# Optimization experiments

Measured on AMD Instinct MI355X. Metric: run time of the kernel, lower is better.

Reference implementation:

```python
import jax, jax.numpy as jnp
import numpy as np

BERT = 178  # BERT_VECTOR_SIZE
WLEN = 20   # letters per word (dim1 = WLEN + BERT)


def _lstm(x, h0, c0, Wih, Whh, bih, bhh):
    """PyTorch-convention LSTM (gate order i,f,g,o). x: [B,T,D] -> outputs [B,T,H]."""
    xg = jnp.einsum('btd,gd->btg', x, Wih) + bih + bhh  # precompute input projections

    def step(carry, xt):
        h, c = carry
        g = xt + h @ Whh.T
        i, f, gg, o = jnp.split(g, 4, axis=-1)
        c = jax.nn.sigmoid(f) * c + jax.nn.sigmoid(i) * jnp.tanh(gg)
        h = jax.nn.sigmoid(o) * jnp.tanh(c)
        return (h, c), h

    _, hs = jax.lax.scan(step, (h0, c0), jnp.swapaxes(xg, 0, 1))
    return jnp.swapaxes(hs, 0, 1)  # [B,T,H]


def setup_inputs() -> dict:
    key = jax.random.key(0)
    ks = jax.random.split(key, 32)
    B, S, L = 32, 64, 50          # batch, sentence_length, number_of_letters
    Hs, Hm, D, O = 128, 256, 128, 32  # secondary_hidden, main_hidden, word_dims, output_size
    NW = B * S
    T = WLEN + BERT
    Din = D + BERT                # sentence LSTM input size = 306
    s = 0.05
    rn = lambda k, sh: jax.random.normal(k, sh, dtype=jnp.float32)
    return {
        'X': rn(ks[0], (B, S, T, L)),
        'h0w': rn(ks[1], (NW, Hs)), 'c0w': rn(ks[2], (NW, Hs)),
        'h0f': rn(ks[3], (B, Hm)), 'c0f': rn(ks[4], (B, Hm)),
        'h0b': rn(ks[5], (B, Hm)), 'c0b': rn(ks[6], (B, Hm)),
        'Wih_w': rn(ks[7], (4 * Hs, L)) * s, 'Whh_w': rn(ks[8], (4 * Hs, Hs)) * s,
        'bih_w': rn(ks[9], (4 * Hs,)) * s, 'bhh_w': rn(ks[10], (4 * Hs,)) * s,
        'Wl': rn(ks[11], (D, Hs)) * s, 'bl': rn(ks[12], (D,)) * s,
        'Wih_f': rn(ks[13], (4 * Hm, Din)) * s, 'Whh_f': rn(ks[14], (4 * Hm, Hm)) * s,
        'bih_f': rn(ks[15], (4 * Hm,)) * s, 'bhh_f': rn(ks[16], (4 * Hm,)) * s,
        'Wih_b': rn(ks[17], (4 * Hm, Din)) * s, 'Whh_b': rn(ks[18], (4 * Hm, Hm)) * s,
        'bih_b': rn(ks[19], (4 * Hm,)) * s, 'bhh_b': rn(ks[20], (4 * Hm,)) * s,
        'Wo': rn(ks[21], (O, 2 * Hm)) * s, 'bo': rn(ks[22], (O,)) * s,
    }


def reference(X, h0w, c0w, h0f, c0f, h0b, c0b,
              Wih_w, Whh_w, bih_w, bhh_w, Wl, bl,
              Wih_f, Whh_f, bih_f, bhh_f,
              Wih_b, Whh_b, bih_b, bhh_b, Wo, bo):
    B, S = X.shape[0], X.shape[1]
    L = X.shape[-1]
    NW = B * S
    Xw = X.reshape(NW, -1, L)            # [NW, WLEN+BERT, L]
    letters = Xw[:, :WLEN, :]            # [NW, WLEN, L]
    bert = Xw[:, -BERT:, 0]              # vectorized replacement of the double loop

    out_w = _lstm(letters, h0w, c0w, Wih_w, Whh_w, bih_w, bhh_w)
    word_rep = out_w[:, -1, :] @ Wl.T + bl        # [NW, D]
    word_rep = jnp.concatenate([word_rep, bert], axis=1)  # [NW, D+BERT]
    sentences = word_rep.reshape(B, S, -1)

    out_f = _lstm(sentences, h0f, c0f, Wih_f, Whh_f, bih_f, bhh_f)
    out_b = _lstm(sentences[:, ::-1, :], h0b, c0b, Wih_b, Whh_b, bih_b, bhh_b)[:, ::-1, :]
    out = jnp.concatenate([out_f, out_b], axis=-1)  # [B, S, 2*Hm]

    words = out.reshape(NW, -1)
    tags = words @ Wo.T + bo
    return jax.nn.softmax(tags, axis=1)
```

## Files before the change

kernel.cpp:

```cpp
#include <hip/hip_runtime.h>
#include <cstdint>
#include <cstddef>

#define DI static __device__ __forceinline__

using half_t  = _Float16;
using half2_t = __attribute__((ext_vector_type(2))) _Float16;
using half8_t = __attribute__((ext_vector_type(8))) _Float16;
using f32x4_t = __attribute__((ext_vector_type(4))) float;

DI uint32_t pack2(float a, float b){ half2_t h; h[0]=(half_t)a; h[1]=(half_t)b; return __builtin_bit_cast(uint32_t,h); }
DI uint16_t f16b(float a){ return __builtin_bit_cast(uint16_t,(half_t)a); }
DI float lo16(uint32_t u){ half2_t h=__builtin_bit_cast(half2_t,u); return (float)h[0]; }
DI float hi16(uint32_t u){ half2_t h=__builtin_bit_cast(half2_t,u); return (float)h[1]; }
DI float fdot2(uint32_t w, uint32_t x, float acc){
  return __builtin_amdgcn_fdot2(__builtin_bit_cast(half2_t,w), __builtin_bit_cast(half2_t,x), acc, false);
}
DI float sigm(float x){ return __builtin_amdgcn_rcpf(1.f + __expf(-x)); }
DI float tanhf_(float x){ return 1.f - 2.f*__builtin_amdgcn_rcpf(__expf(2.f*x)+1.f); }

#define SROW 308
#define HSTR 280

#define N0 32768
#define N1 16384
#define N2 8192
#define N3 512
#define N4 262144
#define N5 313344
#define N6 2048
#define N7 8192
#define N8 364544
#define NTOT (N0+N1+N2+N3+N4+N5+N6+N7+N8)

__global__ void k_prep(const float* __restrict__ X,
                       const float* __restrict__ Wih_w, const float* __restrict__ Whh_w,
                       const float* __restrict__ bih_w, const float* __restrict__ bhh_w,
                       const float* __restrict__ Wl,
                       const float* __restrict__ Wih_f, const float* __restrict__ Whh_f,
                       const float* __restrict__ bih_f, const float* __restrict__ bhh_f,
                       const float* __restrict__ Wih_b, const float* __restrict__ Whh_b,
                       const float* __restrict__ bih_b, const float* __restrict__ bhh_b,
                       const float* __restrict__ Wo,
                       uint32_t* __restrict__ wWsw, uint32_t* __restrict__ wWxw,
                       uint32_t* __restrict__ wWlf, float* __restrict__ wbsw,
                       uint32_t* __restrict__ wWs, uint32_t* __restrict__ wWihs,
                       float* __restrict__ wbss, uint32_t* __restrict__ wWo,
                       float* __restrict__ sent)
{
  for (int i = blockIdx.x*blockDim.x + threadIdx.x; i < NTOT; i += gridDim.x*blockDim.x) {
    int id = i;
    if (id < N0) {
      int kp = id & 63, ng = id >> 6;
      int w = ng>>6, g = (ng>>4)&3, jl = ng&15;
      const float* s = Whh_w + (size_t)(g*128 + w*16 + jl)*128 + 2*kp;
      wWsw[id] = pack2(s[0], s[1]);
    } else if ((id -= N0) < N1) {
      int kp = id & 31, ng = id >> 5;
      int w = ng>>6, g = (ng>>4)&3, jl = ng&15;
      if (kp < 25) {
        const float* s = Wih_w + (size_t)(g*128 + w*16 + jl)*50 + 2*kp;
        wWxw[id] = pack2(s[0], s[1]);
      } else wWxw[id] = 0u;
    } else if ((id -= N1) < N2) {
      int kp = id & 63, d = id >> 6;
      const float* s = Wl + (size_t)d*128 + 2*kp;
      wWlf[id] = pack2(s[0], s[1]);
    } else if ((id -= N2) < N3) {
      int g = id & 3, j = id>>2;
      wbsw[id] = bih_w[g*128+j] + bhh_w[g*128+j];
    } else if ((id -= N3) < N4) {
      int kp = id & 127, ng = (id>>7)&1023, dir = id>>17;
      int w = ng>>7, g = (ng>>5)&3, jl = ng&31;
      int row = g*256 + w*32 + jl;
      const float* s = (dir ? Whh_b : Whh_f) + (size_t)row*256 + 2*kp;
      wWs[id] = pack2(s[0], s[1]);
    } else if ((id -= N4) < N5) {
      int dir = id >= 156672; int r = id - dir*156672;
      int g = r & 3, j = (r>>2)&255, kp = r>>10;
      const float* s = (dir ? Wih_b : Wih_f) + (size_t)(g*256+j)*306 + 2*kp;
      wWihs[id] = pack2(s[0], s[1]);
    } else if ((id -= N5) < N6) {
      int g = id & 3, j = (id>>2)&255, dir = id>>10;
      int row = g*256+j;
      wbss[id] = dir ? (bih_b[row]+bhh_b[row]) : (bih_f[row]+bhh_f[row]);
    } else if ((id -= N6) < N7) {
      int o = id & 31, kp = id>>5;
      const float* s = Wo + (size_t)o*512 + 2*kp;
      wWo[id] = pack2(s[0], s[1]);
    } else { id -= N7;
      int wg = id / 178, ii = id % 178;
      sent[(size_t)wg*SROW + 128 + ii] = X[(size_t)wg*9900 + (20+ii)*50];
    }
  }
}

__global__ __launch_bounds__(512, 2) void k_word(
    const float* __restrict__ X, const float* __restrict__ h0w, const float* __restrict__ c0w,
    const uint32_t* __restrict__ wWsw, const uint32_t* __restrict__ wWxw,
    const float* __restrict__ wbsw, const uint32_t* __restrict__ wWlf,
    const float* __restrict__ bl, float* __restrict__ sent)
{
  __shared__ __align__(16) uint32_t lets[11520];
  __shared__ __align__(16) uint16_t hbuf[2][2176];
  const int tid = threadIdx.x;
  const int wave = tid >> 6, lane = tid & 63;
  const int l15 = lane & 15, l4 = lane >> 4;
  const int wg0 = blockIdx.x * 16;

  uint4 Bh[4][4], Bx[4][2];
  #pragma unroll
  for (int g = 0; g < 4; ++g) {
    int ng = wave*64 + g*16 + l15;
    #pragma unroll
    for (int Kt = 0; Kt < 4; ++Kt) Bh[g][Kt] = *(const uint4*)(wWsw + ng*64 + Kt*16 + l4*4);
    #pragma unroll
    for (int Kt = 0; Kt < 2; ++Kt) Bx[g][Kt] = *(const uint4*)(wWxw + ng*32 + Kt*16 + l4*4);
  }
  for (int i = tid; i < 11520; i += 512) {
    int c = i % 36, mt = i / 36; int m = mt & 15, t = mt >> 4;
    lets[i] = (c < 25) ? pack2(X[(size_t)(wg0+m)*9900 + t*50 + 2*c],
                               X[(size_t)(wg0+m)*9900 + t*50 + 2*c + 1]) : 0u;
  }
  for (int i = tid; i < 2048; i += 512) {
    int m = i >> 7, k = i & 127;
    hbuf[0][m*136 + k] = f16b(h0w[(size_t)(wg0+m)*128 + k]);
  }
  const float4 bs = *(const float4*)(wbsw + (wave*16 + l15)*4);
  float cr[4];
  #pragma unroll
  for (int r = 0; r < 4; ++r) cr[r] = c0w[(size_t)(wg0 + l4*4 + r)*128 + wave*16 + l15];
  __syncthreads();

  uint16_t* hc = hbuf[0];
  uint16_t* hn = hbuf[1];
  const uint16_t* lp = (const uint16_t*)lets;
  #pragma unroll 1
  for (int t = 0; t < 20; ++t) {
    f32x4_t acc[4];
    acc[0] = (f32x4_t){bs.x,bs.x,bs.x,bs.x};
    acc[1] = (f32x4_t){bs.y,bs.y,bs.y,bs.y};
    acc[2] = (f32x4_t){bs.z,bs.z,bs.z,bs.z};
    acc[3] = (f32x4_t){bs.w,bs.w,bs.w,bs.w};
    #pragma unroll
    for (int Kt = 0; Kt < 2; ++Kt) {
      uint4 av = *(const uint4*)(lp + (t*16 + l15)*72 + Kt*32 + l4*8);
      half8_t a = __builtin_bit_cast(half8_t, av);
      #pragma unroll
      for (int g = 0; g < 4; ++g)
        acc[g] = __builtin_amdgcn_mfma_f32_16x16x32_f16(a, __builtin_bit_cast(half8_t, Bx[g][Kt]), acc[g], 0,0,0);
    }
    #pragma unroll
    for (int Kt = 0; Kt < 4; ++Kt) {
      uint4 av = *(const uint4*)(hc + l15*136 + Kt*32 + l4*8);
      half8_t a = __builtin_bit_cast(half8_t, av);
      #pragma unroll
      for (int g = 0; g < 4; ++g)
        acc[g] = __builtin_amdgcn_mfma_f32_16x16x32_f16(a, __builtin_bit_cast(half8_t, Bh[g][Kt]), acc[g], 0,0,0);
    }
    #pragma unroll
    for (int r = 0; r < 4; ++r) {
      float cc = sigm(acc[1][r])*cr[r] + sigm(acc[0][r])*tanhf_(acc[2][r]);
      cr[r] = cc;
      float hh = sigm(acc[3][r])*tanhf_(cc);
      hn[(l4*4+r)*136 + wave*16 + l15] = f16b(hh);
    }
    uint16_t* tp = hc; hc = hn; hn = tp;
    __syncthreads();
  }
  uint4 Bl[4];
  #pragma unroll
  for (int Kt = 0; Kt < 4; ++Kt) Bl[Kt] = *(const uint4*)(wWlf + (wave*16 + l15)*64 + Kt*16 + l4*4);
  f32x4_t a2 = (f32x4_t){0.f,0.f,0.f,0.f};
  #pragma unroll
  for (int Kt = 0; Kt < 4; ++Kt) {
    uint4 av = *(const uint4*)(hc + l15*136 + Kt*32 + l4*8);
    a2 = __builtin_amdgcn_mfma_f32_16x16x32_f16(__builtin_bit_cast(half8_t, av),
                                                __builtin_bit_cast(half8_t, Bl[Kt]), a2, 0,0,0);
  }
  const float blv = bl[wave*16 + l15];
  #pragma unroll
  for (int r = 0; r < 4; ++r)
    sent[(size_t)(wg0 + l4*4 + r)*SROW + wave*16 + l15] = a2[r] + blv;
}

__global__ __launch_bounds__(256) void k_sxg(
    const float* __restrict__ sent, const uint32_t* __restrict__ Wihs,
    const float* __restrict__ bss, uint2* __restrict__ xgq)
{
  __shared__ uint32_t x16[153*8];
  const int tid = threadIdx.x;
  const int dir = blockIdx.x >> 8, rg = blockIdx.x & 255;
  for (int i = tid; i < 153*8; i += 256) {
    int r = i & 7, kp = i >> 3;
    int ot = rg*8 + r; int b = ot >> 6, tt = ot & 63;
    int si = dir ? (63 - tt) : tt;
    const float* s = sent + (size_t)(b*64 + si)*SROW + 2*kp;
    x16[kp*8 + r] = pack2(s[0], s[1]);
  }
  __syncthreads();
  const int j = tid;
  float acc[8][4];
  {
    const float4 b4 = *(const float4*)(bss + (dir*256 + j)*4);
    #pragma unroll
    for (int r = 0; r < 8; ++r) { acc[r][0]=b4.x; acc[r][1]=b4.y; acc[r][2]=b4.z; acc[r][3]=b4.w; }
  }
  for (int kp = 0; kp < 153; ++kp) {
    uint4 wv = *(const uint4*)(Wihs + ((size_t)(dir*153 + kp)*256 + j)*4);
    uint4 xa = *(const uint4*)(x16 + kp*8);
    uint4 xb = *(const uint4*)(x16 + kp*8 + 4);
    uint32_t wa[4] = {wv.x,wv.y,wv.z,wv.w};
    uint32_t xs[8] = {xa.x,xa.y,xa.z,xa.w,xb.x,xb.y,xb.z,xb.w};
    #pragma unroll
    for (int r = 0; r < 8; ++r)
      #pragma unroll
      for (int g = 0; g < 4; ++g) acc[r][g] = fdot2(wa[g], xs[r], acc[r][g]);
  }
  const int w = j >> 5, jh2 = (j >> 4) & 1, l15j = j & 15;
  #pragma unroll
  for (int r = 0; r < 8; ++r) {
    int ot = rg*8 + r; int b = ot >> 6, tt = ot & 63;
    int half = b >> 4, l4m = (b >> 2) & 3, rm = b & 3;
    uint2 v; v.x = pack2(acc[r][0], acc[r][1]); v.y = pack2(acc[r][2], acc[r][3]);
    size_t idx = ((((size_t)(dir*64 + tt)*2 + half)*8 + w)*2 + jh2)*256 + l15j*16 + l4m*4 + rm;
    xgq[idx] = v;
  }
}

__global__ __launch_bounds__(512, 2) void k_srec(
    const uint32_t* __restrict__ Ws, const float* __restrict__ h0f, const float* __restrict__ c0f,
    const float* __restrict__ h0b, const float* __restrict__ c0b,
    const uint2* __restrict__ xgq, uint16_t* __restrict__ outfb)
{
  extern __shared__ char smem[];
  uint16_t* h16a = (uint16_t*)(smem + 131072);
  uint16_t* h16b = h16a + 16*HSTR;
  const int tid = threadIdx.x;
  const int wave = tid >> 6, lane = tid & 63;
  const int dir = blockIdx.x >> 1, half = blockIdx.x & 1, m0 = half * 16;
  const int l15 = lane & 15, l4 = lane >> 4;

  uint4 Breg[8][6];
  #pragma unroll
  for (int Nt = 0; Nt < 8; ++Nt) {
    #pragma unroll
    for (int Kt = 0; Kt < 8; ++Kt) {
      int ng = wave*128 + Nt*16 + l15;
      int kq = Kt*16 + l4*4;
      uint4 v = *(const uint4*)(Ws + (size_t)(dir*1024 + ng)*128 + kq);
      if (Kt < 6) Breg[Nt][Kt] = v;
      else *(uint4*)(smem + (((wave*16 + Nt*2 + (Kt-6))*64 + lane)*16)) = v;
    }
  }
  {
    const float* h0 = dir ? h0b : h0f;
    for (int i = tid; i < 16*256; i += 512) {
      int m = i >> 8, k = i & 255;
      h16a[m*HSTR + k] = f16b(h0[(size_t)(m0+m)*256 + k]);
    }
  }
  float cr[2][4];
  {
    const float* c0 = dir ? c0b : c0f;
    #pragma unroll
    for (int jh = 0; jh < 2; ++jh)
      #pragma unroll
      for (int r = 0; r < 4; ++r) {
        int m = l4*4 + r, jj = wave*32 + jh*16 + l15;
        cr[jh][r] = c0[(size_t)(m0+m)*256 + jj];
      }
  }
  __syncthreads();

  const char* xb = (const char*)xgq + ((size_t)dir*4194304 + (size_t)half*32768)
                 + wave*4096 + l15*128 + l4*32;
  const int s0 = dir ? 63 : 0;
  const int sdelta = dir ? -65536 : 65536;
  char* op = (char*)outfb + (size_t)s0*65536 + half*32768 + dir*16384
           + (l4*4)*512 + wave*64 + l15*2;

  uint16_t* hc = h16a;
  uint16_t* hn = h16b;
  #pragma unroll 1
  for (int t = 0; t < 64; ++t) {
    uint4 xg0a = *(const uint4*)(xb);
    uint4 xg0b = *(const uint4*)(xb + 16);
    uint4 xg1a = *(const uint4*)(xb + 2048);
    uint4 xg1b = *(const uint4*)(xb + 2048 + 16);

    #pragma unroll
    for (int jh = 0; jh < 2; ++jh) {
      const uint4 xga = jh ? xg1a : xg0a;
      const uint4 xgb = jh ? xg1b : xg0b;
      f32x4_t acc[4];
      acc[0] = (f32x4_t){lo16(xga.x), lo16(xga.z), lo16(xgb.x), lo16(xgb.z)};
      acc[1] = (f32x4_t){hi16(xga.x), hi16(xga.z), hi16(xgb.x), hi16(xgb.z)};
      acc[2] = (f32x4_t){lo16(xga.y), lo16(xga.w), lo16(xgb.y), lo16(xgb.w)};
      acc[3] = (f32x4_t){hi16(xga.y), hi16(xga.w), hi16(xgb.y), hi16(xgb.w)};
      #pragma unroll
      for (int Kt = 0; Kt < 8; ++Kt) {
        uint4 av = *(const uint4*)(hc + l15*HSTR + Kt*32 + l4*8);
        half8_t a = __builtin_bit_cast(half8_t, av);
        #pragma unroll
        for (int g = 0; g < 4; ++g) {
          const int Nt = g*2 + jh;
          uint4 bv = (Kt < 6) ? Breg[Nt][Kt]
                   : *(const uint4*)(smem + (((wave*16 + Nt*2 + (Kt-6))*64 + lane)*16));
          acc[g] = __builtin_amdgcn_mfma_f32_16x16x32_f16(a, __builtin_bit_cast(half8_t, bv), acc[g], 0,0,0);
        }
      }
      #pragma unroll
      for (int r = 0; r < 4; ++r) {
        float gi = acc[0][r], gf = acc[1][r], gg = acc[2][r], go = acc[3][r];
        float ef = __expf(-gf), ei = __expf(-gi), eg = __expf(-2.f*gg);
        float pef = 1.f + ef, pei = 1.f + ei, peg = 1.f + eg;
        float num = cr[jh][r]*pei*peg + (1.f - eg)*pef;
        float cc  = num * __builtin_amdgcn_rcpf(pef*pei*peg);
        cr[jh][r] = cc;
        float ec = __expf(-2.f*cc), eo = __expf(-go);
        float hh = (1.f - ec) * __builtin_amdgcn_rcpf((1.f + ec)*(1.f + eo));
        uint16_t hb = f16b(hh);
        hn[(l4*4+r)*HSTR + wave*32 + jh*16 + l15] = hb;
        *(uint16_t*)(op + r*512 + jh*32) = hb;
      }
    }
    { uint16_t* tp = hc; hc = hn; hn = tp; }
    xb += 65536;
    op += sdelta;
    asm volatile("s_waitcnt lgkmcnt(0)\ns_barrier" ::: "memory");
  }
}

__global__ __launch_bounds__(256) void k_tags(
    const uint16_t* __restrict__ outfb, const uint32_t* __restrict__ Wo16,
    const float* __restrict__ bo, float* __restrict__ out)
{
  __shared__ uint32_t xr[8*256];
  const int tid = threadIdx.x;
  const int w0 = blockIdx.x * 8;
  const uint32_t* src = (const uint32_t*)outfb;
  for (int i = tid; i < 2048; i += 256) {
    int w = i >> 8, kp = i & 255;
    int widx = w0 + w;
    int s = widx & 63, q = widx >> 6;
    int half = q >> 4, m = q & 15;
    int dir = kp >> 7, wv = (kp >> 4) & 7, jh = (kp >> 3) & 1, l15h = kp & 7;
    xr[i] = src[s*16384 + half*8192 + dir*4096 + m*128 + wv*16 + jh*8 + l15h];
  }
  __syncthreads();
  const int o = tid & 31, w = tid >> 5;
  float a = bo[o];
  for (int kp = 0; kp < 256; ++kp)
    a = fdot2(Wo16[kp*32 + o], xr[w*256 + kp], a);
  float mx = a;
  #pragma unroll
  for (int off = 16; off; off >>= 1) mx = fmaxf(mx, __shfl_xor(mx, off, 32));
  float e = __expf(a - mx);
  float ssum = e;
  #pragma unroll
  for (int off = 16; off; off >>= 1) ssum += __shfl_xor(ssum, off, 32);
  out[(size_t)(w0+w)*32 + o] = e * __builtin_amdgcn_rcpf(ssum);
}

extern "C" void kernel_launch(void* const* d_in, const int* in_sizes, int n_in,
                              void* d_out, int out_size, void* d_ws, size_t ws_size,
                              hipStream_t stream) {
  const float* X     = (const float*)d_in[0];
  const float* h0w   = (const float*)d_in[1];
  const float* c0w   = (const float*)d_in[2];
  const float* h0f   = (const float*)d_in[3];
  const float* c0f   = (const float*)d_in[4];
  const float* h0b   = (const float*)d_in[5];
  const float* c0b   = (const float*)d_in[6];
  const float* Wih_w = (const float*)d_in[7];
  const float* Whh_w = (const float*)d_in[8];
  const float* bih_w = (const float*)d_in[9];
  const float* bhh_w = (const float*)d_in[10];
  const float* Wl    = (const float*)d_in[11];
  const float* bl    = (const float*)d_in[12];
  const float* Wih_f = (const float*)d_in[13];
  const float* Whh_f = (const float*)d_in[14];
  const float* bih_f = (const float*)d_in[15];
  const float* bhh_f = (const float*)d_in[16];
  const float* Wih_b = (const float*)d_in[17];
  const float* Whh_b = (const float*)d_in[18];
  const float* bih_b = (const float*)d_in[19];
  const float* bhh_b = (const float*)d_in[20];
  const float* Wo    = (const float*)d_in[21];
  const float* bo    = (const float*)d_in[22];

  char* ws = (char*)d_ws;
  uint32_t* wWsw  = (uint32_t*)(ws + 0);
  uint32_t* wWxw  = (uint32_t*)(ws + 131072);
  uint32_t* wWlf  = (uint32_t*)(ws + 196608);
  float*    wbsw  = (float*)   (ws + 229376);
  uint32_t* wWs   = (uint32_t*)(ws + 231424);
  uint32_t* wWihs = (uint32_t*)(ws + 1280000);
  float*    wbss  = (float*)   (ws + 2533376);
  uint32_t* wWo   = (uint32_t*)(ws + 2541568);
  float*    sent  = (float*)   (ws + 2574336);
  uint2*    xgq   = (uint2*)   (ws + 5097472);
  uint16_t* outfb = (uint16_t*)(ws + 13486080);

  hipFuncSetAttribute((const void*)k_srec, hipFuncAttributeMaxDynamicSharedMemorySize, 148992);

  k_prep<<<2048, 256, 0, stream>>>(X, Wih_w, Whh_w, bih_w, bhh_w, Wl, Wih_f, Whh_f, bih_f, bhh_f,
                                   Wih_b, Whh_b, bih_b, bhh_b, Wo,
                                   wWsw, wWxw, wWlf, wbsw, wWs, wWihs, wbss, wWo, sent);
  k_word<<<128, 512, 0, stream>>>(X, h0w, c0w, wWsw, wWxw, wbsw, wWlf, bl, sent);
  k_sxg<<<512, 256, 0, stream>>>(sent, wWihs, wbss, xgq);
  k_srec<<<4, 512, 148992, stream>>>(wWs, h0f, c0f, h0b, c0b, xgq, outfb);
  k_tags<<<256, 256, 0, stream>>>(outfb, wWo, bo, (float*)d_out);
}
```

Measured before the change: 308.3 us.

## Restructure sentence LSTM recurrence to four waves with 64 units each

The sentence recurrence kernel now runs 256 threads per block instead of 512, so each wave owns 64 hidden units and does four gate passes per timestep. The recurrent weight packing, the input-gate (xgq) layout and the output layout are all re-laid out to match, and k_tags reads the new output layout. Gate-input loads are interleaved with the passes to overlap global latency with the MFMA chains. The aim is cheaper per-step barriers and more per-wave work between syncs. In exchange, each SIMD has a single wave to hide latency, and register pressure is high: 96 uint4 weights are held in registers per thread, which risks spilling.

```diff
diff --git a/kernel.cpp b/kernel.cpp
--- a/kernel.cpp
+++ b/kernel.cpp
@@ -71,8 +71,8 @@
       wbsw[id] = bih_w[g*128+j] + bhh_w[g*128+j];
     } else if ((id -= N3) < N4) {
       int kp = id & 127, ng = (id>>7)&1023, dir = id>>17;
-      int w = ng>>7, g = (ng>>5)&3, jl = ng&31;
-      int row = g*256 + w*32 + jl;
+      int w = (ng>>8)&3, g = (ng>>6)&3, p = (ng>>4)&3, jl = ng&15;
+      int row = g*256 + w*64 + p*16 + jl;
       const float* s = (dir ? Whh_b : Whh_f) + (size_t)row*256 + 2*kp;
       wWs[id] = pack2(s[0], s[1]);
     } else if ((id -= N4) < N5) {
@@ -217,18 +217,19 @@
       #pragma unroll
       for (int g = 0; g < 4; ++g) acc[r][g] = fdot2(wa[g], xs[r], acc[r][g]);
   }
-  const int w = j >> 5, jh2 = (j >> 4) & 1, l15j = j & 15;
+  const int w = j >> 6, p = (j >> 4) & 3, l15j = j & 15;
   #pragma unroll
   for (int r = 0; r < 8; ++r) {
     int ot = rg*8 + r; int b = ot >> 6, tt = ot & 63;
-    int half = b >> 4, l4m = (b >> 2) & 3, rm = b & 3;
+    int half = b >> 4, m = b & 15;
+    int l4m = m >> 2, rm = m & 3;
     uint2 v; v.x = pack2(acc[r][0], acc[r][1]); v.y = pack2(acc[r][2], acc[r][3]);
-    size_t idx = ((((size_t)(dir*64 + tt)*2 + half)*8 + w)*2 + jh2)*256 + l15j*16 + l4m*4 + rm;
+    size_t idx = ((((size_t)(dir*64 + tt)*2 + half)*4 + w)*4 + p)*256 + l15j*16 + l4m*4 + rm;
     xgq[idx] = v;
   }
 }
 
-__global__ __launch_bounds__(512, 2) void k_srec(
+__global__ __launch_bounds__(256, 1) void k_srec(
     const uint32_t* __restrict__ Ws, const float* __restrict__ h0f, const float* __restrict__ c0f,
     const float* __restrict__ h0b, const float* __restrict__ c0b,
     const uint2* __restrict__ xgq, uint16_t* __restrict__ outfb)
@@ -241,95 +242,113 @@
   const int dir = blockIdx.x >> 1, half = blockIdx.x & 1, m0 = half * 16;
   const int l15 = lane & 15, l4 = lane >> 4;
 
-  uint4 Breg[8][6];
-  #pragma unroll
-  for (int Nt = 0; Nt < 8; ++Nt) {
-    #pragma unroll
-    for (int Kt = 0; Kt < 8; ++Kt) {
-      int ng = wave*128 + Nt*16 + l15;
-      int kq = Kt*16 + l4*4;
-      uint4 v = *(const uint4*)(Ws + (size_t)(dir*1024 + ng)*128 + kq);
-      if (Kt < 6) Breg[Nt][Kt] = v;
-      else *(uint4*)(smem + (((wave*16 + Nt*2 + (Kt-6))*64 + lane)*16)) = v;
-    }
-  }
+  uint4 Breg[4][4][6];
+  #pragma unroll
+  for (int g = 0; g < 4; ++g)
+    #pragma unroll
+    for (int p = 0; p < 4; ++p) {
+      int ng = wave*256 + g*64 + p*16 + l15;
+      #pragma unroll
+      for (int Kt = 0; Kt < 8; ++Kt) {
+        uint4 v = *(const uint4*)(Ws + (size_t)(dir*1024 + ng)*128 + Kt*16 + l4*4);
+        if (Kt < 6) Breg[g][p][Kt] = v;
+        else *(uint4*)(smem + (((wave*32 + (g*4+p)*2 + (Kt-6))*64 + lane)*16)) = v;
+      }
+    }
   {
     const float* h0 = dir ? h0b : h0f;
-    for (int i = tid; i < 16*256; i += 512) {
+    for (int i = tid; i < 16*256; i += 256) {
       int m = i >> 8, k = i & 255;
       h16a[m*HSTR + k] = f16b(h0[(size_t)(m0+m)*256 + k]);
     }
   }
-  float cr[2][4];
+  f32x4_t cr0, cr1, cr2, cr3;
   {
     const float* c0 = dir ? c0b : c0f;
     #pragma unroll
-    for (int jh = 0; jh < 2; ++jh)
-      #pragma unroll
-      for (int r = 0; r < 4; ++r) {
-        int m = l4*4 + r, jj = wave*32 + jh*16 + l15;
-        cr[jh][r] = c0[(size_t)(m0+m)*256 + jj];
-      }
+    for (int r = 0; r < 4; ++r) {
+      cr0[r] = c0[(size_t)(m0 + l4*4 + r)*256 + wave*64 + 0*16 + l15];
+      cr1[r] = c0[(size_t)(m0 + l4*4 + r)*256 + wave*64 + 1*16 + l15];
+      cr2[r] = c0[(size_t)(m0 + l4*4 + r)*256 + wave*64 + 2*16 + l15];
+      cr3[r] = c0[(size_t)(m0 + l4*4 + r)*256 + wave*64 + 3*16 + l15];
+    }
   }
   __syncthreads();
 
-  const char* xb = (const char*)xgq + ((size_t)dir*4194304 + (size_t)half*32768)
-                 + wave*4096 + l15*128 + l4*32;
+  const char* xb = (const char*)xgq + (size_t)dir*4194304 + half*32768
+                 + wave*8192 + l15*128 + l4*32;
   const int s0 = dir ? 63 : 0;
-  const int sdelta = dir ? -65536 : 65536;
-  char* op = (char*)outfb + (size_t)s0*65536 + half*32768 + dir*16384
-           + (l4*4)*512 + wave*64 + l15*2;
+  const int sdelta = dir ? -32768 : 32768;
+  char* op = (char*)outfb + (size_t)s0*32768 + half*16384 + dir*8192
+           + (l4*4)*512 + wave*128 + l15*2;
 
   uint16_t* hc = h16a;
   uint16_t* hn = h16b;
+
+#define XLOAD(P, XA, XB_) { XA = *(const uint4*)(xb + (P)*2048); XB_ = *(const uint4*)(xb + (P)*2048 + 16); }
+
+#define PASS(P, XA, XB_, CRV) {                                                          \
+    f32x4_t a0, a1, a2, a3;                                                              \
+    a0 = (f32x4_t){lo16(XA.x), lo16(XA.z), lo16(XB_.x), lo16(XB_.z)};                    \
+    a1 = (f32x4_t){hi16(XA.x), hi16(XA.z), hi16(XB_.x), hi16(XB_.z)};                    \
+    a2 = (f32x4_t){lo16(XA.y), lo16(XA.w), lo16(XB_.y), lo16(XB_.w)};                    \
+    a3 = (f32x4_t){hi16(XA.y), hi16(XA.w), hi16(XB_.y), hi16(XB_.w)};                    \
+    _Pragma("unroll")                                                                    \
+    for (int Kh = 0; Kh < 2; ++Kh) {                                                     \
+      uint4 av0 = *(const uint4*)(hc + l15*HSTR + (Kh*4+0)*32 + l4*8);                   \
+      uint4 av1 = *(const uint4*)(hc + l15*HSTR + (Kh*4+1)*32 + l4*8);                   \
+      uint4 av2 = *(const uint4*)(hc + l15*HSTR + (Kh*4+2)*32 + l4*8);                   \
+      uint4 av3 = *(const uint4*)(hc + l15*HSTR + (Kh*4+3)*32 + l4*8);                   \
+      _Pragma("unroll")                                                                  \
+      for (int g = 0; g < 4; ++g) {                                                      \
+        f32x4_t* ac = (g==0)?&a0:(g==1)?&a1:(g==2)?&a2:&a3;                              \
+        _Pragma("unroll")                                                                \
+        for (int Kq = 0; Kq < 4; ++Kq) {                                                 \
+          const int Kt = Kh*4 + Kq;                                                      \
+          uint4 av = (Kq==0)?av0:(Kq==1)?av1:(Kq==2)?av2:av3;                            \
+          uint4 bv;                                                                      \
+          if (Kt < 6) bv = Breg[g][P][Kt];                                               \
+          else bv = *(const uint4*)(smem + (((wave*32 + (g*4+(P))*2 + (Kt-6))*64 + lane)*16)); \
+          *ac = __builtin_amdgcn_mfma_f32_16x16x32_f16(__builtin_bit_cast(half8_t, av),  \
+                 __builtin_bit_cast(half8_t, bv), *ac, 0,0,0);                           \
+        }                                                                                \
+      }                                                                                  \
+    }                                                                                    \
+    _Pragma("unroll")                                                                    \
+    for (int r = 0; r < 4; ++r) {                                                        \
+      float gi = a0[r], gf = a1[r], gg = a2[r], go = a3[r];                              \
+      float ef = __expf(-gf), ei = __expf(-gi), eg = __expf(-2.f*gg);                    \
+      float pef = 1.f + ef, pei = 1.f + ei, peg = 1.f + eg;                              \
+      float num = CRV[r]*pei*peg + (1.f - eg)*pef;                                       \
+      float cc  = num * __builtin_amdgcn_rcpf(pef*pei*peg);                              \
+      CRV[r] = cc;                                                                       \
+      float ec = __expf(-2.f*cc), eo = __expf(-go);                                      \
+      float hh = (1.f - ec) * __builtin_amdgcn_rcpf((1.f + ec)*(1.f + eo));              \
+      uint16_t hb = f16b(hh);                                                            \
+      hn[(l4*4+r)*HSTR + wave*64 + (P)*16 + l15] = hb;                                   \
+      *(uint16_t*)(op + (P)*32 + r*512) = hb;                                            \
+    }                                                                                    \
+  }
+
+  uint4 xpa, xpb, xqa, xqb;
   #pragma unroll 1
   for (int t = 0; t < 64; ++t) {
-    uint4 xg0a = *(const uint4*)(xb);
-    uint4 xg0b = *(const uint4*)(xb + 16);
-    uint4 xg1a = *(const uint4*)(xb + 2048);
-    uint4 xg1b = *(const uint4*)(xb + 2048 + 16);
-
-    #pragma unroll
-    for (int jh = 0; jh < 2; ++jh) {
-      const uint4 xga = jh ? xg1a : xg0a;
-      const uint4 xgb = jh ? xg1b : xg0b;
-      f32x4_t acc[4];
-      acc[0] = (f32x4_t){lo16(xga.x), lo16(xga.z), lo16(xgb.x), lo16(xgb.z)};
-      acc[1] = (f32x4_t){hi16(xga.x), hi16(xga.z), hi16(xgb.x), hi16(xgb.z)};
-      acc[2] = (f32x4_t){lo16(xga.y), lo16(xga.w), lo16(xgb.y), lo16(xgb.w)};
-      acc[3] = (f32x4_t){hi16(xga.y), hi16(xga.w), hi16(xgb.y), hi16(xgb.w)};
-      #pragma unroll
-      for (int Kt = 0; Kt < 8; ++Kt) {
-        uint4 av = *(const uint4*)(hc + l15*HSTR + Kt*32 + l4*8);
-        half8_t a = __builtin_bit_cast(half8_t, av);
-        #pragma unroll
-        for (int g = 0; g < 4; ++g) {
-          const int Nt = g*2 + jh;
-          uint4 bv = (Kt < 6) ? Breg[Nt][Kt]
-                   : *(const uint4*)(smem + (((wave*16 + Nt*2 + (Kt-6))*64 + lane)*16));
-          acc[g] = __builtin_amdgcn_mfma_f32_16x16x32_f16(a, __builtin_bit_cast(half8_t, bv), acc[g], 0,0,0);
-        }
-      }
-      #pragma unroll
-      for (int r = 0; r < 4; ++r) {
-        float gi = acc[0][r], gf = acc[1][r], gg = acc[2][r], go = acc[3][r];
-        float ef = __expf(-gf), ei = __expf(-gi), eg = __expf(-2.f*gg);
-        float pef = 1.f + ef, pei = 1.f + ei, peg = 1.f + eg;
-        float num = cr[jh][r]*pei*peg + (1.f - eg)*pef;
-        float cc  = num * __builtin_amdgcn_rcpf(pef*pei*peg);
-        cr[jh][r] = cc;
-        float ec = __expf(-2.f*cc), eo = __expf(-go);
-        float hh = (1.f - ec) * __builtin_amdgcn_rcpf((1.f + ec)*(1.f + eo));
-        uint16_t hb = f16b(hh);
-        hn[(l4*4+r)*HSTR + wave*32 + jh*16 + l15] = hb;
-        *(uint16_t*)(op + r*512 + jh*32) = hb;
-      }
-    }
+    XLOAD(0, xpa, xpb);
+    XLOAD(1, xqa, xqb);
+    PASS(0, xpa, xpb, cr0);
+    XLOAD(2, xpa, xpb);
+    PASS(1, xqa, xqb, cr1);
+    XLOAD(3, xqa, xqb);
+    PASS(2, xpa, xpb, cr2);
+    PASS(3, xqa, xqb, cr3);
+
     { uint16_t* tp = hc; hc = hn; hn = tp; }
     xb += 65536;
     op += sdelta;
     asm volatile("s_waitcnt lgkmcnt(0)\ns_barrier" ::: "memory");
   }
+#undef PASS
+#undef XLOAD
 }
 
 __global__ __launch_bounds__(256) void k_tags(
@@ -345,8 +364,8 @@
     int widx = w0 + w;
     int s = widx & 63, q = widx >> 6;
     int half = q >> 4, m = q & 15;
-    int dir = kp >> 7, wv = (kp >> 4) & 7, jh = (kp >> 3) & 1, l15h = kp & 7;
-    xr[i] = src[s*16384 + half*8192 + dir*4096 + m*128 + wv*16 + jh*8 + l15h];
+    int dir = kp >> 7, jp = kp & 127;
+    xr[i] = src[s*8192 + half*4096 + dir*2048 + m*128 + jp];
   }
   __syncthreads();
   const int o = tid & 31, w = tid >> 5;
@@ -410,6 +429,6 @@
                                    wWsw, wWxw, wWlf, wbsw, wWs, wWihs, wbss, wWo, sent);
   k_word<<<128, 512, 0, stream>>>(X, h0w, c0w, wWsw, wWxw, wbsw, wWlf, bl, sent);
   k_sxg<<<512, 256, 0, stream>>>(sent, wWihs, wbss, xgq);
-  k_srec<<<4, 512, 148992, stream>>>(wWs, h0f, c0f, h0b, c0b, xgq, outfb);
+  k_srec<<<4, 256, 148992, stream>>>(wWs, h0f, c0f, h0b, c0b, xgq, outfb);
   k_tags<<<256, 256, 0, stream>>>(outfb, wWo, bo, (float*)d_out);
 }
```

Result: slower. 463.0 us (+50.2%).

## Split sentence LSTM recurrence across 16 waves per block instead of 8

Applied to the files above, without the earlier changes.

The sentence-level recurrent kernel now launches 1024 threads per block, so each wave owns 16 hidden units instead of 32. Per-wave register weights, the xg and output layouts, and the tags gather indexing are rearranged to match. The aim is to halve the serial MFMA and gate work per wave on each of the 64 dependent timesteps. The cost is more waves joining each per-step barrier, plus register pressure limits under 1024-thread launch bounds.

```diff
diff --git a/kernel.cpp b/kernel.cpp
--- a/kernel.cpp
+++ b/kernel.cpp
@@ -71,8 +71,8 @@
       wbsw[id] = bih_w[g*128+j] + bhh_w[g*128+j];
     } else if ((id -= N3) < N4) {
       int kp = id & 127, ng = (id>>7)&1023, dir = id>>17;
-      int w = ng>>7, g = (ng>>5)&3, jl = ng&31;
-      int row = g*256 + w*32 + jl;
+      int w = ng>>6, g = (ng>>4)&3, jl = ng&15;
+      int row = g*256 + w*16 + jl;
       const float* s = (dir ? Whh_b : Whh_f) + (size_t)row*256 + 2*kp;
       wWs[id] = pack2(s[0], s[1]);
     } else if ((id -= N4) < N5) {
@@ -217,117 +217,106 @@
       #pragma unroll
       for (int g = 0; g < 4; ++g) acc[r][g] = fdot2(wa[g], xs[r], acc[r][g]);
   }
-  const int w = j >> 5, jh2 = (j >> 4) & 1, l15j = j & 15;
+  const int w = j >> 4, l15j = j & 15;
   #pragma unroll
   for (int r = 0; r < 8; ++r) {
     int ot = rg*8 + r; int b = ot >> 6, tt = ot & 63;
-    int half = b >> 4, l4m = (b >> 2) & 3, rm = b & 3;
+    int half = b >> 4, m = b & 15;
+    int l4m = m >> 2, rm = m & 3;
     uint2 v; v.x = pack2(acc[r][0], acc[r][1]); v.y = pack2(acc[r][2], acc[r][3]);
-    size_t idx = ((((size_t)(dir*64 + tt)*2 + half)*8 + w)*2 + jh2)*256 + l15j*16 + l4m*4 + rm;
+    size_t idx = (((size_t)(dir*64 + tt)*2 + half)*16 + w)*256 + l15j*16 + l4m*4 + rm;
     xgq[idx] = v;
   }
 }
 
-__global__ __launch_bounds__(512, 2) void k_srec(
+__global__ __launch_bounds__(1024, 1) void k_srec(
     const uint32_t* __restrict__ Ws, const float* __restrict__ h0f, const float* __restrict__ c0f,
     const float* __restrict__ h0b, const float* __restrict__ c0b,
     const uint2* __restrict__ xgq, uint16_t* __restrict__ outfb)
 {
   extern __shared__ char smem[];
-  uint16_t* h16a = (uint16_t*)(smem + 131072);
-  uint16_t* h16b = h16a + 16*HSTR;
   const int tid = threadIdx.x;
   const int wave = tid >> 6, lane = tid & 63;
   const int dir = blockIdx.x >> 1, half = blockIdx.x & 1, m0 = half * 16;
   const int l15 = lane & 15, l4 = lane >> 4;
 
-  uint4 Breg[8][6];
-  #pragma unroll
-  for (int Nt = 0; Nt < 8; ++Nt) {
+  uint4 Breg[4][6];
+  #pragma unroll
+  for (int g = 0; g < 4; ++g) {
+    int ng = wave*64 + g*16 + l15;
     #pragma unroll
     for (int Kt = 0; Kt < 8; ++Kt) {
-      int ng = wave*128 + Nt*16 + l15;
-      int kq = Kt*16 + l4*4;
-      uint4 v = *(const uint4*)(Ws + (size_t)(dir*1024 + ng)*128 + kq);
-      if (Kt < 6) Breg[Nt][Kt] = v;
-      else *(uint4*)(smem + (((wave*16 + Nt*2 + (Kt-6))*64 + lane)*16)) = v;
+      uint4 v = *(const uint4*)(Ws + (size_t)(dir*1024 + ng)*128 + Kt*16 + l4*4);
+      if (Kt < 6) Breg[g][Kt] = v;
+      else *(uint4*)(smem + (((wave*8 + g*2 + (Kt-6))*64 + lane)*16)) = v;
     }
   }
   {
+    uint16_t* h16a = (uint16_t*)(smem + 131072);
     const float* h0 = dir ? h0b : h0f;
-    for (int i = tid; i < 16*256; i += 512) {
+    for (int i = tid; i < 16*256; i += 1024) {
       int m = i >> 8, k = i & 255;
       h16a[m*HSTR + k] = f16b(h0[(size_t)(m0+m)*256 + k]);
     }
   }
-  float cr[2][4];
+  float cr[4];
   {
     const float* c0 = dir ? c0b : c0f;
     #pragma unroll
-    for (int jh = 0; jh < 2; ++jh)
-      #pragma unroll
-      for (int r = 0; r < 4; ++r) {
-        int m = l4*4 + r, jj = wave*32 + jh*16 + l15;
-        cr[jh][r] = c0[(size_t)(m0+m)*256 + jj];
-      }
+    for (int r = 0; r < 4; ++r)
+      cr[r] = c0[(size_t)(m0 + l4*4 + r)*256 + wave*16 + l15];
   }
   __syncthreads();
 
-  const char* xb = (const char*)xgq + ((size_t)dir*4194304 + (size_t)half*32768)
-                 + wave*4096 + l15*128 + l4*32;
-  const int s0 = dir ? 63 : 0;
-  const int sdelta = dir ? -65536 : 65536;
-  char* op = (char*)outfb + (size_t)s0*65536 + half*32768 + dir*16384
-           + (l4*4)*512 + wave*64 + l15*2;
-
-  uint16_t* hc = h16a;
-  uint16_t* hn = h16b;
+  const uint32_t xlane = wave*2048 + l15*128 + l4*32;
+  const char* xbase = (const char*)xgq + (size_t)dir*4194304 + half*32768;
+  const uint32_t olane = (l4*4)*512 + wave*32 + l15*2;
+  char* obase = (char*)outfb + half*16384 + dir*8192;
+  const uint32_t aoff = l15*HSTR + l4*8;
+
   #pragma unroll 1
   for (int t = 0; t < 64; ++t) {
-    uint4 xg0a = *(const uint4*)(xb);
-    uint4 xg0b = *(const uint4*)(xb + 16);
-    uint4 xg1a = *(const uint4*)(xb + 2048);
-    uint4 xg1b = *(const uint4*)(xb + 2048 + 16);
-
-    #pragma unroll
-    for (int jh = 0; jh < 2; ++jh) {
-      const uint4 xga = jh ? xg1a : xg0a;
-      const uint4 xgb = jh ? xg1b : xg0b;
-      f32x4_t acc[4];
-      acc[0] = (f32x4_t){lo16(xga.x), lo16(xga.z), lo16(xgb.x), lo16(xgb.z)};
-      acc[1] = (f32x4_t){hi16(xga.x), hi16(xga.z), hi16(xgb.x), hi16(xgb.z)};
-      acc[2] = (f32x4_t){lo16(xga.y), lo16(xga.w), lo16(xgb.y), lo16(xgb.w)};
-      acc[3] = (f32x4_t){hi16(xga.y), hi16(xga.w), hi16(xgb.y), hi16(xgb.w)};
+    const char* xp = xbase + (size_t)t*65536 + xlane;
+    uint4 xa  = *(const uint4*)(xp);
+    uint4 xb2 = *(const uint4*)(xp + 16);
+    f32x4_t a0 = (f32x4_t){lo16(xa.x), lo16(xa.z), lo16(xb2.x), lo16(xb2.z)};
+    f32x4_t a1 = (f32x4_t){hi16(xa.x), hi16(xa.z), hi16(xb2.x), hi16(xb2.z)};
+    f32x4_t a2 = (f32x4_t){lo16(xa.y), lo16(xa.w), lo16(xb2.y), lo16(xb2.w)};
+    f32x4_t a3 = (f32x4_t){hi16(xa.y), hi16(xa.w), hi16(xb2.y), hi16(xb2.w)};
+
+    const uint16_t* hc = (const uint16_t*)(smem + 131072 + (t & 1)*8960);
+    uint16_t* hn = (uint16_t*)(smem + 131072 + ((t & 1) ^ 1)*8960);
+
+    #pragma unroll
+    for (int Kt = 0; Kt < 8; ++Kt) {
+      uint4 av = *(const uint4*)(hc + aoff + Kt*32);
+      half8_t a = __builtin_bit_cast(half8_t, av);
       #pragma unroll
-      for (int Kt = 0; Kt < 8; ++Kt) {
-        uint4 av = *(const uint4*)(hc + l15*HSTR + Kt*32 + l4*8);
-        half8_t a = __builtin_bit_cast(half8_t, av);
-        #pragma unroll
-        for (int g = 0; g < 4; ++g) {
-          const int Nt = g*2 + jh;
-          uint4 bv = (Kt < 6) ? Breg[Nt][Kt]
-                   : *(const uint4*)(smem + (((wave*16 + Nt*2 + (Kt-6))*64 + lane)*16));
-          acc[g] = __builtin_amdgcn_mfma_f32_16x16x32_f16(a, __builtin_bit_cast(half8_t, bv), acc[g], 0,0,0);
-        }
+      for (int g = 0; g < 4; ++g) {
+        uint4 bv;
+        if (Kt < 6) bv = Breg[g][Kt];
+        else bv = *(const uint4*)(smem + (((wave*8 + g*2 + (Kt-6))*64 + lane)*16));
+        f32x4_t* ac = (g==0)?&a0:(g==1)?&a1:(g==2)?&a2:&a3;
+        *ac = __builtin_amdgcn_mfma_f32_16x16x32_f16(a, __builtin_bit_cast(half8_t, bv), *ac, 0,0,0);
       }
-      #pragma unroll
-      for (int r = 0; r < 4; ++r) {
-        float gi = acc[0][r], gf = acc[1][r], gg = acc[2][r], go = acc[3][r];
-        float ef = __expf(-gf), ei = __expf(-gi), eg = __expf(-2.f*gg);
-        float pef = 1.f + ef, pei = 1.f + ei, peg = 1.f + eg;
-        float num = cr[jh][r]*pei*peg + (1.f - eg)*pef;
-        float cc  = num * __builtin_amdgcn_rcpf(pef*pei*peg);
-        cr[jh][r] = cc;
-        float ec = __expf(-2.f*cc), eo = __expf(-go);
-        float hh = (1.f - ec) * __builtin_amdgcn_rcpf((1.f + ec)*(1.f + eo));
-        uint16_t hb = f16b(hh);
-        hn[(l4*4+r)*HSTR + wave*32 + jh*16 + l15] = hb;
-        *(uint16_t*)(op + r*512 + jh*32) = hb;
-      }
-    }
-    { uint16_t* tp = hc; hc = hn; hn = tp; }
-    xb += 65536;
-    op += sdelta;
+    }
+
+    const int s = dir ? (63 - t) : t;
+    char* op = obase + (size_t)s*32768 + olane;
+    #pragma unroll
+    for (int r = 0; r < 4; ++r) {
+      float gi = a0[r], gf = a1[r], gg = a2[r], go = a3[r];
+      float ef = __expf(-gf), ei = __expf(-gi), eg = __expf(-2.f*gg);
+      float pef = 1.f + ef, pei = 1.f + ei, peg = 1.f + eg;
+      float num = cr[r]*pei*peg + (1.f - eg)*pef;
+      float cc  = num * __builtin_amdgcn_rcpf(pef*pei*peg);
+      cr[r] = cc;
+      float ec = __expf(-2.f*cc), eo = __expf(-go);
+      float hh = (1.f - ec) * __builtin_amdgcn_rcpf((1.f + ec)*(1.f + eo));
+      uint16_t hb = f16b(hh);
+      hn[(l4*4+r)*HSTR + wave*16 + l15] = hb;
+      *(uint16_t*)(op + r*512) = hb;
+    }
     asm volatile("s_waitcnt lgkmcnt(0)\ns_barrier" ::: "memory");
   }
 }
@@ -345,8 +334,8 @@
     int widx = w0 + w;
     int s = widx & 63, q = widx >> 6;
     int half = q >> 4, m = q & 15;
-    int dir = kp >> 7, wv = (kp >> 4) & 7, jh = (kp >> 3) & 1, l15h = kp & 7;
-    xr[i] = src[s*16384 + half*8192 + dir*4096 + m*128 + wv*16 + jh*8 + l15h];
+    int dir = kp >> 7, jp = kp & 127;
+    xr[i] = src[s*8192 + half*4096 + dir*2048 + m*128 + jp];
   }
   __syncthreads();
   const int o = tid & 31, w = tid >> 5;
@@ -410,6 +399,6 @@
                                    wWsw, wWxw, wWlf, wbsw, wWs, wWihs, wbss, wWo, sent);
   k_word<<<128, 512, 0, stream>>>(X, h0w, c0w, wWsw, wWxw, wbsw, wWlf, bl, sent);
   k_sxg<<<512, 256, 0, stream>>>(sent, wWihs, wbss, xgq);
-  k_srec<<<4, 512, 148992, stream>>>(wWs, h0f, c0f, h0b, c0b, xgq, outfb);
+  k_srec<<<4, 1024, 148992, stream>>>(wWs, h0f, c0f, h0b, c0b, xgq, outfb);
   k_tags<<<256, 256, 0, stream>>>(outfb, wWo, bo, (float*)d_out);
 }
```

Result: slower. 349.5 us (+13.3%).

## Prefetch next-step input gates and merge both gate halves into one MFMA pass

Applied to the files above, without the earlier changes.

Each step of the sentence LSTM recurrence now issues the global loads for the next timestep's precomputed input gates right after the MFMA loop, so their latency overlaps the activation math and the barrier. The two jh halves are merged into a single K loop over all 8 N tiles with 8 accumulators, so each A fragment is read from LDS once instead of twice per step. This raises register pressure (8 accumulators plus 4 prefetch registers on top of 48 uint4 held B tiles), which could cause spills or lower occupancy. The final iteration prefetches one timestep past the end, which relies on that memory being readable.

```diff
diff --git a/kernel.cpp b/kernel.cpp
--- a/kernel.cpp
+++ b/kernel.cpp
@@ -247,8 +247,7 @@
     #pragma unroll
     for (int Kt = 0; Kt < 8; ++Kt) {
       int ng = wave*128 + Nt*16 + l15;
-      int kq = Kt*16 + l4*4;
-      uint4 v = *(const uint4*)(Ws + (size_t)(dir*1024 + ng)*128 + kq);
+      uint4 v = *(const uint4*)(Ws + (size_t)(dir*1024 + ng)*128 + Kt*16 + l4*4);
       if (Kt < 6) Breg[Nt][Kt] = v;
       else *(uint4*)(smem + (((wave*16 + Nt*2 + (Kt-6))*64 + lane)*16)) = v;
     }
@@ -266,53 +265,62 @@
     #pragma unroll
     for (int jh = 0; jh < 2; ++jh)
       #pragma unroll
-      for (int r = 0; r < 4; ++r) {
-        int m = l4*4 + r, jj = wave*32 + jh*16 + l15;
-        cr[jh][r] = c0[(size_t)(m0+m)*256 + jj];
-      }
+      for (int r = 0; r < 4; ++r)
+        cr[jh][r] = c0[(size_t)(m0 + l4*4 + r)*256 + wave*32 + jh*16 + l15];
   }
   __syncthreads();
 
-  const char* xb = (const char*)xgq + ((size_t)dir*4194304 + (size_t)half*32768)
-                 + wave*4096 + l15*128 + l4*32;
+  const char* xbase = (const char*)xgq + (size_t)dir*4194304 + half*32768;
+  const uint32_t xlane = wave*4096 + l15*128 + l4*32;
   const int s0 = dir ? 63 : 0;
   const int sdelta = dir ? -65536 : 65536;
-  char* op = (char*)outfb + (size_t)s0*65536 + half*32768 + dir*16384
-           + (l4*4)*512 + wave*64 + l15*2;
+  const char* obase = (const char*)outfb + (size_t)s0*65536 + half*32768 + dir*16384;
+  const uint32_t olane = (l4*4)*512 + wave*64 + l15*2;
+  const uint32_t aoff = l15*HSTR + l4*8;
 
   uint16_t* hc = h16a;
   uint16_t* hn = h16b;
+
+  uint4 p0 = *(const uint4*)(xbase + xlane);
+  uint4 p1 = *(const uint4*)(xbase + xlane + 16);
+  uint4 p2 = *(const uint4*)(xbase + xlane + 2048);
+  uint4 p3 = *(const uint4*)(xbase + xlane + 2064);
+
   #pragma unroll 1
   for (int t = 0; t < 64; ++t) {
-    uint4 xg0a = *(const uint4*)(xb);
-    uint4 xg0b = *(const uint4*)(xb + 16);
-    uint4 xg1a = *(const uint4*)(xb + 2048);
-    uint4 xg1b = *(const uint4*)(xb + 2048 + 16);
+    f32x4_t acc[8];
+    acc[0] = (f32x4_t){lo16(p0.x), lo16(p0.z), lo16(p1.x), lo16(p1.z)};
+    acc[2] = (f32x4_t){hi16(p0.x), hi16(p0.z), hi16(p1.x), hi16(p1.z)};
+    acc[4] = (f32x4_t){lo16(p0.y), lo16(p0.w), lo16(p1.y), lo16(p1.w)};
+    acc[6] = (f32x4_t){hi16(p0.y), hi16(p0.w), hi16(p1.y), hi16(p1.w)};
+    acc[1] = (f32x4_t){lo16(p2.x), lo16(p2.z), lo16(p3.x), lo16(p3.z)};
+    acc[3] = (f32x4_t){hi16(p2.x), hi16(p2.z), hi16(p3.x), hi16(p3.z)};
+    acc[5] = (f32x4_t){lo16(p2.y), lo16(p2.w), lo16(p3.y), lo16(p3.w)};
+    acc[7] = (f32x4_t){hi16(p2.y), hi16(p2.w), hi16(p3.y), hi16(p3.w)};
+
+    #pragma unroll
+    for (int Kt = 0; Kt < 8; ++Kt) {
+      uint4 av = *(const uint4*)(hc + aoff + Kt*32);
+      half8_t a = __builtin_bit_cast(half8_t, av);
+      #pragma unroll
+      for (int Nt = 0; Nt < 8; ++Nt) {
+        uint4 bv;
+        if (Kt < 6) bv = Breg[Nt][Kt];
+        else bv = *(const uint4*)(smem + (((wave*16 + Nt*2 + (Kt-6))*64 + lane)*16));
+        acc[Nt] = __builtin_amdgcn_mfma_f32_16x16x32_f16(a, __builtin_bit_cast(half8_t, bv), acc[Nt], 0,0,0);
+      }
+    }
+
+    p0 = *(const uint4*)(xbase + xlane + 65536);
+    p1 = *(const uint4*)(xbase + xlane + 65536 + 16);
+    p2 = *(const uint4*)(xbase + xlane + 65536 + 2048);
+    p3 = *(const uint4*)(xbase + xlane + 65536 + 2064);
 
     #pragma unroll
     for (int jh = 0; jh < 2; ++jh) {
-      const uint4 xga = jh ? xg1a : xg0a;
-      const uint4 xgb = jh ? xg1b : xg0b;
-      f32x4_t acc[4];
-      acc[0] = (f32x4_t){lo16(xga.x), lo16(xga.z), lo16(xgb.x), lo16(xgb.z)};
-      acc[1] = (f32x4_t){hi16(xga.x), hi16(xga.z), hi16(xgb.x), hi16(xgb.z)};
-      acc[2] = (f32x4_t){lo16(xga.y), lo16(xga.w), lo16(xgb.y), lo16(xgb.w)};
-      acc[3] = (f32x4_t){hi16(xga.y), hi16(xga.w), hi16(xgb.y), hi16(xgb.w)};
-      #pragma unroll
-      for (int Kt = 0; Kt < 8; ++Kt) {
-        uint4 av = *(const uint4*)(hc + l15*HSTR + Kt*32 + l4*8);
-        half8_t a = __builtin_bit_cast(half8_t, av);
-        #pragma unroll
-        for (int g = 0; g < 4; ++g) {
-          const int Nt = g*2 + jh;
-          uint4 bv = (Kt < 6) ? Breg[Nt][Kt]
-                   : *(const uint4*)(smem + (((wave*16 + Nt*2 + (Kt-6))*64 + lane)*16));
-          acc[g] = __builtin_amdgcn_mfma_f32_16x16x32_f16(a, __builtin_bit_cast(half8_t, bv), acc[g], 0,0,0);
-        }
-      }
       #pragma unroll
       for (int r = 0; r < 4; ++r) {
-        float gi = acc[0][r], gf = acc[1][r], gg = acc[2][r], go = acc[3][r];
+        float gi = acc[0+jh][r], gf = acc[2+jh][r], gg = acc[4+jh][r], go = acc[6+jh][r];
         float ef = __expf(-gf), ei = __expf(-gi), eg = __expf(-2.f*gg);
         float pef = 1.f + ef, pei = 1.f + ei, peg = 1.f + eg;
         float num = cr[jh][r]*pei*peg + (1.f - eg)*pef;
@@ -322,12 +330,12 @@
         float hh = (1.f - ec) * __builtin_amdgcn_rcpf((1.f + ec)*(1.f + eo));
         uint16_t hb = f16b(hh);
         hn[(l4*4+r)*HSTR + wave*32 + jh*16 + l15] = hb;
-        *(uint16_t*)(op + r*512 + jh*32) = hb;
+        *(uint16_t*)(obase + olane + r*512 + jh*32) = hb;
       }
     }
     { uint16_t* tp = hc; hc = hn; hn = tp; }
-    xb += 65536;
-    op += sdelta;
+    xbase += 65536;
+    obase += sdelta;
     asm volatile("s_waitcnt lgkmcnt(0)\ns_barrier" ::: "memory");
   }
 }
```

New measurement: 310.7 us. No clear change (+0.8%).
